# Performance work log

Hardware: AMD Instinct MI355X
Metric: run time of the kernel (lower is better)

The kernel has to match this reference:

```python
import jax, jax.numpy as jnp
import numpy as np

B, T, D, H = 4, 2048, 1024, 16
HS = D // H
EPS = 1e-5

def layer_norm(x, g, b):
    mu = jnp.mean(x, axis=-1, keepdims=True)
    var = jnp.var(x, axis=-1, keepdims=True)
    return (x - mu) * jax.lax.rsqrt(var + EPS) * g + b

def setup_inputs() -> dict:
    key = jax.random.key(0)
    ks = jax.random.split(key, 12)
    s_in = 1.0 / np.sqrt(D)
    s_ff = 1.0 / np.sqrt(4 * D)
    return {
        "x": jax.random.normal(ks[0], (B, T, D), jnp.float32),
        "Wq": jax.random.uniform(ks[1], (H, D, HS), jnp.float32, -s_in, s_in),
        "Wk": jax.random.uniform(ks[2], (H, D, HS), jnp.float32, -s_in, s_in),
        "Wv": jax.random.uniform(ks[3], (H, D, HS), jnp.float32, -s_in, s_in),
        "Wp": jax.random.uniform(ks[4], (D, D), jnp.float32, -s_in, s_in),
        "bp": jax.random.uniform(ks[5], (D,), jnp.float32, -s_in, s_in),
        "W1": jax.random.uniform(ks[6], (D, 4 * D), jnp.float32, -s_in, s_in),
        "b1": jax.random.uniform(ks[7], (4 * D,), jnp.float32, -s_in, s_in),
        "W2": jax.random.uniform(ks[8], (4 * D, D), jnp.float32, -s_ff, s_ff),
        "b2": jax.random.uniform(ks[9], (D,), jnp.float32, -s_ff, s_ff),
        "g1": jnp.ones((D,), jnp.float32),
        "be1": jnp.zeros((D,), jnp.float32),
        "g2": jnp.ones((D,), jnp.float32),
        "be2": jnp.zeros((D,), jnp.float32),
    }

def reference(x, Wq, Wk, Wv, Wp, bp, W1, b1, W2, b2, g1, be1, g2, be2):
    # pre-LN (note: residual uses the NORMALIZED tensor, matching original code)
    h = layer_norm(x, g1, be1)                          # [B,T,D]
    q = jnp.einsum('btd,hdk->bhtk', h, Wq)              # [B,H,T,hs]
    k = jnp.einsum('btd,hdk->bhtk', h, Wk)
    v = jnp.einsum('btd,hdk->bhtk', h, Wv)
    # NOTE: original scales by embedding_size**-0.5, not head_size
    scores = jnp.einsum('bhtk,bhsk->bhts', q, k) * (D ** -0.5)
    causal = jnp.tril(jnp.ones((T, T), bool))
    scores = jnp.where(causal, scores, -jnp.inf)
    att = jax.nn.softmax(scores, axis=-1)               # [B,H,T,T]
    o = jnp.einsum('bhts,bhsk->bhtk', att, v)
    o = o.transpose(0, 2, 1, 3).reshape(B, T, D)        # concat heads
    o = o @ Wp + bp
    x2 = h + o
    h2 = layer_norm(x2, g2, be2)
    ff = jax.nn.relu(h2 @ W1 + b1) @ W2 + b2
    return h2 + ff
```

## Files before the change

kernel.cpp:

```cpp
#include <hip/hip_runtime.h>
#include <hip/hip_bf16.h>

#define Bq 4
#define Tq 2048
#define Dq 1024
#define Hq 16
#define HSq 64
#define EPSq 1e-5f

typedef __attribute__((ext_vector_type(8))) short s16x8;
typedef __attribute__((ext_vector_type(4))) float f32x4;

#define GLL16(g, l)                                                        \
    __builtin_amdgcn_global_load_lds(                                      \
        (const __attribute__((address_space(1))) void*)(g),                \
        (__attribute__((address_space(3))) void*)(l), 16, 0, 0)

__device__ __forceinline__ ushort f2bf(float f) {
    union { float f; unsigned u; } x; x.f = f;
    unsigned r = x.u + 0x7fffu + ((x.u >> 16) & 1u);
    return (ushort)(r >> 16);
}

__global__ __launch_bounds__(256) void ln_bf16(const float* __restrict__ x,
                                               const float* __restrict__ g,
                                               const float* __restrict__ bb,
                                               float* __restrict__ y,
                                               ushort* __restrict__ y16) {
    __shared__ float sdata[8];
    int row = blockIdx.x;
    const float4* xr = (const float4*)(x + (size_t)row * Dq);
    float4 v = xr[threadIdx.x];
    float s  = v.x + v.y + v.z + v.w;
    float ss = v.x*v.x + v.y*v.y + v.z*v.z + v.w*v.w;
    for (int off = 32; off; off >>= 1) {
        s  += __shfl_down(s,  off);
        ss += __shfl_down(ss, off);
    }
    int lane = threadIdx.x & 63, wid = threadIdx.x >> 6;
    if (lane == 0) { sdata[wid] = s; sdata[4 + wid] = ss; }
    __syncthreads();
    if (threadIdx.x == 0) {
        sdata[0] = sdata[0] + sdata[1] + sdata[2] + sdata[3];
        sdata[4] = sdata[4] + sdata[5] + sdata[6] + sdata[7];
    }
    __syncthreads();
    float mu  = sdata[0] * (1.f / Dq);
    float var = sdata[4] * (1.f / Dq) - mu * mu;
    float inv = rsqrtf(var + EPSq);
    float4 gv = ((const float4*)g)[threadIdx.x];
    float4 bv = ((const float4*)bb)[threadIdx.x];
    float4 o;
    o.x = (v.x - mu) * inv * gv.x + bv.x;
    o.y = (v.y - mu) * inv * gv.y + bv.y;
    o.z = (v.z - mu) * inv * gv.z + bv.z;
    o.w = (v.w - mu) * inv * gv.w + bv.w;
    ((float4*)(y + (size_t)row * Dq))[threadIdx.x] = o;
    ushort4 u4;
    u4.x = f2bf(o.x); u4.y = f2bf(o.y); u4.z = f2bf(o.z); u4.w = f2bf(o.w);
    *(ushort4*)(y16 + (size_t)row * Dq + threadIdx.x * 4) = u4;
}

__global__ __launch_bounds__(256) void repack_qkvT(const float* __restrict__ Wqm,
                                                   const float* __restrict__ Wkm,
                                                   const float* __restrict__ Wvm,
                                                   ushort* __restrict__ out) {
    __shared__ float tile[64][65];
    int bid = blockIdx.x;
    int p  = bid >> 8;
    int hh = (bid >> 4) & 15;
    int kt = bid & 15;
    int k0 = kt * 64;
    const float* W = (p == 0) ? Wqm : ((p == 1) ? Wkm : Wvm);
    float scale = (p == 0) ? 0.03125f : 1.0f;
    int j  = threadIdx.x & 63;
    int i0 = threadIdx.x >> 6;
#pragma unroll
    for (int r = 0; r < 16; r++) {
        int i = r * 4 + i0;
        tile[i][j] = W[(size_t)hh * (Dq * HSq) + (size_t)(k0 + i) * HSq + j];
    }
    __syncthreads();
#pragma unroll
    for (int r = 0; r < 16; r++) {
        int i = r * 4 + i0;
        out[(size_t)(p * Dq + hh * HSq + i) * Dq + k0 + j] = f2bf(tile[j][i] * scale);
    }
}

__global__ __launch_bounds__(256) void transpose_cvt(const float* __restrict__ in,
                                                     ushort* __restrict__ out,
                                                     int K, int N) {
    __shared__ float tile[64][65];
    int k0 = blockIdx.y * 64, n0 = blockIdx.x * 64;
    int j  = threadIdx.x & 63;
    int i0 = threadIdx.x >> 6;
#pragma unroll
    for (int r = 0; r < 16; r++) {
        int i = r * 4 + i0;
        tile[i][j] = in[(size_t)(k0 + i) * N + n0 + j];
    }
    __syncthreads();
#pragma unroll
    for (int r = 0; r < 16; r++) {
        int i = r * 4 + i0;
        out[(size_t)(n0 + i) * K + k0 + j] = f2bf(tile[j][i]);
    }
}

template<int BNF>
__global__ __launch_bounds__(256, (BNF == 8) ? 2 : 4)
void gemm_bf16(const ushort* __restrict__ A,
               const ushort* __restrict__ BT,
               const float* __restrict__ bias,
               const float* __restrict__ resid,
               void* __restrict__ Cp,
               ushort* __restrict__ vtg,
               int M, int N, int K,
               int lda, int ldc,
               int relu, int out_bf16,
               int sr) {
    constexpr int BN = BNF * 32;
    constexpr int BSLOT = BN * 32;
    __shared__ ushort lds[2 * 4096 + 3 * BSLOT];
    ushort* Alds = lds;
    ushort* Blds = lds + 2 * 4096;

    int tid = threadIdx.x;
    int w = tid >> 6, lane = tid & 63;
    int lm = lane & 15, quad = lane >> 4;
    int wm = w >> 1, wn = w & 1;

    int bid = blockIdx.x;
    int mtiles = M >> 7, ntiles = N / BN;
    int rt, ct;
    if (mtiles == 64 && (gridDim.x & 7) == 0) {
        int xcd = bid & 7, l = bid >> 3;
        int band = l / (sr * ntiles);
        int rem  = l - band * sr * ntiles;
        ct = rem / sr;
        int srt = rem - ct * sr;
        rt = xcd * 8 + band * sr + srt;
    } else {
        rt = bid % mtiles; ct = bid / mtiles;
    }
    int row0 = rt << 7, col0 = ct * BN;

    int srow = w * 16 + (lane >> 2);
    int schk = (lane & 3) ^ ((lane >> 3) & 3);
    const ushort* pA = A  + (size_t)(row0 + srow) * lda + schk * 8;
    const ushort* pB = BT + (size_t)(col0 + srow) * K  + schk * 8;

    auto stageA = [&](int slot, int t) {
        GLL16(pA + (size_t)t * 32, Alds + slot * 4096 + w * 512);
        GLL16(pA + (size_t)t * 32 + (size_t)64 * lda, Alds + slot * 4096 + 2048 + w * 512);
    };
    auto stageBh = [&](int slot, int t, int h) {
        const ushort* g = pB + (size_t)t * 32 + (size_t)(h * 128) * K;
        ushort* l = Blds + slot * BSLOT + h * 4096 + w * 512;
        GLL16(g, l);
        GLL16(g + (size_t)64 * K, l + 2048);
    };

    int qsw = (quad ^ ((lm >> 1) & 3)) * 8;

    f32x4 zero = {0.f, 0.f, 0.f, 0.f};
    f32x4 acc[4][BNF];
#pragma unroll
    for (int i = 0; i < 4; i++)
#pragma unroll
        for (int jj = 0; jj < BNF; jj++) acc[i][jj] = zero;

    int nkt = K >> 5;

    stageA(0, 0);
    stageBh(0, 0, 0);
    if constexpr (BNF == 8) stageBh(0, 0, 1);
    stageBh(1, 1, 0);
    if constexpr (BNF == 8) stageBh(1, 1, 1);
    __builtin_amdgcn_sched_barrier(0);
    if constexpr (BNF == 8) { asm volatile("s_waitcnt vmcnt(4)" ::: "memory"); }
    else                    { asm volatile("s_waitcnt vmcnt(2)" ::: "memory"); }
    __builtin_amdgcn_s_barrier();
    __builtin_amdgcn_sched_barrier(0);

    int sA = 0, sB = 0;
    for (int t = 0; t < nkt; ++t) {
        const bool stA = (t + 1 < nkt);
        const bool stB = (t + 2 < nkt);
        int sB2 = sB + 2; if (sB2 >= 3) sB2 -= 3;
        const ushort* Ab = Alds + sA * 4096  + (wm * 64 + lm) * 32;
        const ushort* Bb = Blds + sB * BSLOT + (wn * (BNF * 16) + lm) * 32;
        s16x8 a[4], b0[BNF / 2], b1[BNF / 2];

        if (stA) stageA(sA ^ 1, t + 1);
        if (stB) {
            stageBh(sB2, t + 2, 0);
            if constexpr (BNF == 8) stageBh(sB2, t + 2, 1);
        }
        __builtin_amdgcn_sched_barrier(0);

#pragma unroll
        for (int m = 0; m < 4; m++)
            a[m] = *(const s16x8*)(Ab + m * 512 + qsw);
#pragma unroll
        for (int nf = 0; nf < BNF / 2; nf++)
            b0[nf] = *(const s16x8*)(Bb + nf * 512 + qsw);
        __builtin_amdgcn_s_setprio(1);
#pragma unroll
        for (int m = 0; m < 4; m++)
#pragma unroll
            for (int nf = 0; nf < BNF / 2; nf++)
                acc[m][nf] = __builtin_amdgcn_mfma_f32_16x16x32_bf16(a[m], b0[nf], acc[m][nf], 0, 0, 0);
#pragma unroll
        for (int nf = 0; nf < BNF / 2; nf++)
            b1[nf] = *(const s16x8*)(Bb + (nf + BNF / 2) * 512 + qsw);
#pragma unroll
        for (int m = 0; m < 4; m++)
#pragma unroll
            for (int nf = 0; nf < BNF / 2; nf++)
                acc[m][nf + BNF / 2] = __builtin_amdgcn_mfma_f32_16x16x32_bf16(a[m], b1[nf], acc[m][nf + BNF / 2], 0, 0, 0);
        __builtin_amdgcn_s_setprio(0);

        __builtin_amdgcn_sched_barrier(0);
        if (stB) {
            if constexpr (BNF == 8) { asm volatile("s_waitcnt vmcnt(4)" ::: "memory"); }
            else                    { asm volatile("s_waitcnt vmcnt(2)" ::: "memory"); }
        } else if (stA) {
            asm volatile("s_waitcnt vmcnt(0)" ::: "memory");
        }
        if (stA) {
            __builtin_amdgcn_s_barrier();
            __builtin_amdgcn_sched_barrier(0);
        }

        sA ^= 1;
        sB += 1; if (sB >= 3) sB -= 3;
    }

    if (vtg && col0 >= 2048) {
#pragma unroll
        for (int m = 0; m < 4; m++) {
            int r0 = row0 + wm * 64 + m * 16 + quad * 4;
            int bb = r0 >> 11;
            int t  = r0 & (Tq - 1);
#pragma unroll
            for (int nf = 0; nf < BNF; nf++) {
                int hsg = col0 - 2048 + wn * (BNF * 16) + nf * 16 + lm;
                ushort4 u;
                u.x = f2bf(acc[m][nf][0]);
                u.y = f2bf(acc[m][nf][1]);
                u.z = f2bf(acc[m][nf][2]);
                u.w = f2bf(acc[m][nf][3]);
                *(ushort4*)(vtg + ((size_t)(bb * Hq + (hsg >> 6)) * HSq + (hsg & 63)) * Tq + t) = u;
            }
        }
        return;
    }

    float bcol[BNF];
#pragma unroll
    for (int nf = 0; nf < BNF; nf++)
        bcol[nf] = bias ? bias[col0 + wn * (BNF * 16) + nf * 16 + lm] : 0.f;

#pragma unroll
    for (int m = 0; m < 4; m++) {
#pragma unroll
        for (int p = 0; p < 4; p++) {
            int r = row0 + wm * 64 + m * 16 + quad * 4 + p;
#pragma unroll
            for (int nf = 0; nf < BNF; nf++) {
                int cc = col0 + wn * (BNF * 16) + nf * 16 + lm;
                float v = acc[m][nf][p] + bcol[nf];
                if (relu) v = fmaxf(v, 0.f);
                if (resid) v += resid[(size_t)r * ldc + cc];
                if (out_bf16) ((ushort*)Cp)[(size_t)r * ldc + cc] = f2bf(v);
                else          ((float*)Cp)[(size_t)r * ldc + cc] = v;
            }
        }
    }
}

__global__ __launch_bounds__(256) void attn_mfma(const ushort* __restrict__ qkv,
                                                 const ushort* __restrict__ VtG,
                                                 ushort* __restrict__ o16) {
    __shared__ ushort Ks[64 * 72];
    __shared__ ushort Vt[64 * 64];
    __shared__ ushort Ps[4 * 16 * 72];

    int gid = blockIdx.x;
    int b  = gid >> 8;
    int hh = (gid >> 4) & 15;
    int pr = (gid + 7 * b) & 15;
    int qa = pr;
    int qb = 31 - pr;

    int tid = threadIdx.x;
    int w = tid >> 6, lane = tid & 63;
    int lm = lane & 15, quad = lane >> 4;

    const int rs3 = 3 * Dq;
    const ushort* qbase = qkv + (size_t)(b * Tq) * rs3 + hh * HSq;
    int qra = qa * 64 + w * 16 + lm;
    int qrb = qb * 64 + w * 16 + lm;
    s16x8 aqa0 = *(const s16x8*)(qbase + (size_t)qra * rs3 + quad * 8);
    s16x8 aqa1 = *(const s16x8*)(qbase + (size_t)qra * rs3 + 32 + quad * 8);
    s16x8 aqb0 = *(const s16x8*)(qbase + (size_t)qrb * rs3 + quad * 8);
    s16x8 aqb1 = *(const s16x8*)(qbase + (size_t)qrb * rs3 + 32 + quad * 8);

    s16x8 ones;
#pragma unroll
    for (int j = 0; j < 8; j++) ones[j] = (short)0x3F80;

    f32x4 zero = {0.f, 0.f, 0.f, 0.f};
    f32x4 oa[4], ob[4];
#pragma unroll
    for (int nt = 0; nt < 4; nt++) { oa[nt] = zero; ob[nt] = zero; }
    f32x4 la = zero, lb = zero;

    const ushort* kbase = qkv + (size_t)(b * Tq) * rs3 + Dq + hh * HSq;
    const ushort* vtb = VtG + (size_t)((b * Hq + hh) * HSq) * Tq;

    int kr = tid >> 3, kc = (tid & 7) * 8;
    int vh = tid >> 2, vc0 = (tid & 3) * 8;
    int vswz = (((vh >> 3) ^ vh) & 7) << 3;

    s16x8 kp0 = *(const s16x8*)(kbase + (size_t)kr * rs3 + kc);
    s16x8 kp1 = *(const s16x8*)(kbase + (size_t)(kr + 32) * rs3 + kc);
    s16x8 vp0 = *(const s16x8*)(vtb + (size_t)vh * Tq + vc0);
    s16x8 vp1 = *(const s16x8*)(vtb + (size_t)vh * Tq + vc0 + 32);

    auto do_tile = [&](const s16x8& aq0, const s16x8& aq1,
                       f32x4 (&o_acc)[4], f32x4& l_acc, int diag) {
        f32x4 sacc[4];
#pragma unroll
        for (int kt2 = 0; kt2 < 4; kt2++) {
            const ushort* krp = &Ks[(kt2 * 16 + lm) * 72 + quad * 8];
            s16x8 bk0 = *(const s16x8*)krp;
            s16x8 bk1 = *(const s16x8*)(krp + 32);
            f32x4 t = __builtin_amdgcn_mfma_f32_16x16x32_bf16(aq0, bk0, zero, 0, 0, 0);
            sacc[kt2] = __builtin_amdgcn_mfma_f32_16x16x32_bf16(aq1, bk1, t, 0, 0, 0);
        }
        if (diag) {
#pragma unroll
            for (int kt2 = 0; kt2 < 4; kt2++)
#pragma unroll
                for (int r = 0; r < 4; r++)
                    if (kt2 * 16 + lm > w * 16 + quad * 4 + r) sacc[kt2][r] = -1e30f;
        }
#pragma unroll
        for (int kt2 = 0; kt2 < 4; kt2++)
#pragma unroll
            for (int r = 0; r < 4; r++)
                Ps[(w * 16 + quad * 4 + r) * 72 + kt2 * 16 + lm] = f2bf(__expf(sacc[kt2][r]));

        s16x8 ap0 = *(const s16x8*)&Ps[(w * 16 + lm) * 72 + quad * 8];
        s16x8 ap1 = *(const s16x8*)&Ps[(w * 16 + lm) * 72 + 32 + quad * 8];

#pragma unroll
        for (int nt = 0; nt < 4; nt++) {
            int n = nt * 16 + lm;
            int swz = (((n >> 3) ^ n) & 7) << 3;
            s16x8 bv0 = *(const s16x8*)&Vt[n * 64 + ((quad * 8) ^ swz)];
            s16x8 bv1 = *(const s16x8*)&Vt[n * 64 + ((32 + quad * 8) ^ swz)];
            f32x4 t = __builtin_amdgcn_mfma_f32_16x16x32_bf16(ap0, bv0, o_acc[nt], 0, 0, 0);
            o_acc[nt] = __builtin_amdgcn_mfma_f32_16x16x32_bf16(ap1, bv1, t, 0, 0, 0);
        }
        f32x4 t2 = __builtin_amdgcn_mfma_f32_16x16x32_bf16(ap0, ones, l_acc, 0, 0, 0);
        l_acc = __builtin_amdgcn_mfma_f32_16x16x32_bf16(ap1, ones, t2, 0, 0, 0);
    };

    for (int kt = 0; kt <= qb; kt++) {
        __syncthreads();
        *(s16x8*)&Ks[kr * 72 + kc] = kp0;
        *(s16x8*)&Ks[(kr + 32) * 72 + kc] = kp1;
        *(s16x8*)&Vt[vh * 64 + (vc0 ^ vswz)] = vp0;
        *(s16x8*)&Vt[vh * 64 + ((vc0 + 32) ^ vswz)] = vp1;
        __syncthreads();

        if (kt < qb) {
            const ushort* kb = kbase + (size_t)((kt + 1) * 64) * rs3;
            kp0 = *(const s16x8*)(kb + (size_t)kr * rs3 + kc);
            kp1 = *(const s16x8*)(kb + (size_t)(kr + 32) * rs3 + kc);
            const ushort* vb = vtb + (size_t)vh * Tq + (kt + 1) * 64;
            vp0 = *(const s16x8*)(vb + vc0);
            vp1 = *(const s16x8*)(vb + vc0 + 32);
        }

        do_tile(aqb0, aqb1, ob, lb, kt == qb);
        if (kt <= qa)
            do_tile(aqa0, aqa1, oa, la, kt == qa);
    }

#pragma unroll
    for (int r = 0; r < 4; r++) {
        float inva = 1.f / la[r];
        float invb = 1.f / lb[r];
        size_t rowa = (size_t)(b * Tq + qa * 64 + w * 16 + quad * 4 + r);
        size_t rowb = (size_t)(b * Tq + qb * 64 + w * 16 + quad * 4 + r);
#pragma unroll
        for (int nt = 0; nt < 4; nt++) {
            o16[rowa * Dq + hh * HSq + nt * 16 + lm] = f2bf(oa[nt][r] * inva);
            o16[rowb * Dq + hh * HSq + nt * 16 + lm] = f2bf(ob[nt][r] * invb);
        }
    }
}

extern "C" void kernel_launch(void* const* d_in, const int* in_sizes, int n_in,
                              void* d_out, int out_size, void* d_ws, size_t ws_size,
                              hipStream_t stream) {
    const float* x   = (const float*)d_in[0];
    const float* Wq  = (const float*)d_in[1];
    const float* Wk  = (const float*)d_in[2];
    const float* Wv  = (const float*)d_in[3];
    const float* Wp  = (const float*)d_in[4];
    const float* bp  = (const float*)d_in[5];
    const float* W1  = (const float*)d_in[6];
    const float* b1  = (const float*)d_in[7];
    const float* W2  = (const float*)d_in[8];
    const float* b2  = (const float*)d_in[9];
    const float* g1  = (const float*)d_in[10];
    const float* be1 = (const float*)d_in[11];
    const float* g2  = (const float*)d_in[12];
    const float* be2 = (const float*)d_in[13];
    float* out = (float*)d_out;

    const size_t MB = 1u << 20;
    char* ws = (char*)d_ws;
    float*  slotA = (float*)(ws);
    ushort* qkv   = (ushort*)(ws + 32 * MB);
    float*  pbuf  = (float*)(ws + 32 * MB);
    ushort* u16   = (ushort*)(ws + 32 * MB);
    ushort* slotC = (ushort*)(ws + 96 * MB);
    ushort* WqkvT = (ushort*)(ws + 112 * MB);
    ushort* WpT   = (ushort*)(ws + 118 * MB);
    ushort* W1T   = (ushort*)(ws + 120 * MB);
    ushort* W2T   = (ushort*)(ws + 128 * MB);
    ushort* VtG   = (ushort*)(ws + 136 * MB);

    const int rows = Bq * Tq;

    hipLaunchKernelGGL(repack_qkvT, dim3(3 * 16 * 16), dim3(256), 0, stream, Wq, Wk, Wv, WqkvT);
    hipLaunchKernelGGL(transpose_cvt, dim3(Dq / 64, Dq / 64), dim3(256), 0, stream, Wp, WpT, Dq, Dq);
    hipLaunchKernelGGL(transpose_cvt, dim3(4 * Dq / 64, Dq / 64), dim3(256), 0, stream, W1, W1T, Dq, 4 * Dq);
    hipLaunchKernelGGL(transpose_cvt, dim3(Dq / 64, 4 * Dq / 64), dim3(256), 0, stream, W2, W2T, 4 * Dq, Dq);

    hipLaunchKernelGGL(ln_bf16, dim3(rows), dim3(256), 0, stream, x, g1, be1, slotA, slotC);
    hipLaunchKernelGGL(gemm_bf16<8>, dim3((rows / 128) * (3 * Dq / 256)), dim3(256), 0, stream,
                       slotC, WqkvT, (const float*)nullptr, (const float*)nullptr, (void*)qkv, VtG,
                       rows, 3 * Dq, Dq, Dq, 3 * Dq, 0, 1, 8);
    hipLaunchKernelGGL(attn_mfma, dim3(Bq * Hq * 16), dim3(256), 0, stream, qkv, VtG, slotC);
    hipLaunchKernelGGL(gemm_bf16<4>, dim3((rows / 128) * (Dq / 128)), dim3(256), 0, stream,
                       slotC, WpT, bp, slotA, (void*)pbuf, (ushort*)nullptr,
                       rows, Dq, Dq, Dq, Dq, 0, 0, 8);
    hipLaunchKernelGGL(ln_bf16, dim3(rows), dim3(256), 0, stream, pbuf, g2, be2, slotA, slotC);
    hipLaunchKernelGGL(gemm_bf16<8>, dim3((rows / 128) * (4 * Dq / 256)), dim3(256), 0, stream,
                       slotC, W1T, b1, (const float*)nullptr, (void*)u16, (ushort*)nullptr,
                       rows, 4 * Dq, Dq, Dq, 4 * Dq, 1, 1, 8);
    hipLaunchKernelGGL(gemm_bf16<4>, dim3((rows / 128) * (Dq / 128)), dim3(256), 0, stream,
                       u16, W2T, b2, slotA, (void*)out, (ushort*)nullptr,
                       rows, Dq, 4 * Dq, 4 * Dq, Dq, 0, 0, 4);
}
```

Baseline: 503.7 us.

## Process two query-tile pairs per 512-thread attention block sharing K/V tiles

Each attention workgroup now has 8 waves split into two groups. Each group handles its own pair of query tiles (pr/31-pr and 15-pr/16+pr), and both groups share every K/V tile staged in LDS. This halves the grid and the global K/V loads per query, and each thread loads one vector of K and one of V per step instead of two. The cost is imbalance: the group with the shorter pair sits idle at the block barriers while the other finishes, and the larger block may reduce occupancy.

```diff
diff --git a/kernel.cpp b/kernel.cpp
--- a/kernel.cpp
+++ b/kernel.cpp
@@ -281,28 +281,31 @@
     }
 }
 
-__global__ __launch_bounds__(256) void attn_mfma(const ushort* __restrict__ qkv,
+__global__ __launch_bounds__(512) void attn_mfma(const ushort* __restrict__ qkv,
                                                  const ushort* __restrict__ VtG,
                                                  ushort* __restrict__ o16) {
     __shared__ ushort Ks[64 * 72];
     __shared__ ushort Vt[64 * 64];
-    __shared__ ushort Ps[4 * 16 * 72];
+    __shared__ ushort Ps[8 * 16 * 72];
 
     int gid = blockIdx.x;
-    int b  = gid >> 8;
-    int hh = (gid >> 4) & 15;
-    int pr = (gid + 7 * b) & 15;
-    int qa = pr;
-    int qb = 31 - pr;
+    int b  = gid >> 7;
+    int hh = (gid >> 3) & 15;
+    int pr = (gid + 3 * b) & 7;
 
     int tid = threadIdx.x;
     int w = tid >> 6, lane = tid & 63;
+    int g = w >> 2, wl = w & 3;
     int lm = lane & 15, quad = lane >> 4;
+
+    int qa = g ? (15 - pr) : pr;
+    int qb = g ? (16 + pr) : (31 - pr);
+    int qbmax = 31 - pr;
 
     const int rs3 = 3 * Dq;
     const ushort* qbase = qkv + (size_t)(b * Tq) * rs3 + hh * HSq;
-    int qra = qa * 64 + w * 16 + lm;
-    int qrb = qb * 64 + w * 16 + lm;
+    int qra = qa * 64 + wl * 16 + lm;
+    int qrb = qb * 64 + wl * 16 + lm;
     s16x8 aqa0 = *(const s16x8*)(qbase + (size_t)qra * rs3 + quad * 8);
     s16x8 aqa1 = *(const s16x8*)(qbase + (size_t)qra * rs3 + 32 + quad * 8);
     s16x8 aqb0 = *(const s16x8*)(qbase + (size_t)qrb * rs3 + quad * 8);
@@ -322,13 +325,11 @@
     const ushort* vtb = VtG + (size_t)((b * Hq + hh) * HSq) * Tq;
 
     int kr = tid >> 3, kc = (tid & 7) * 8;
-    int vh = tid >> 2, vc0 = (tid & 3) * 8;
+    int vh = tid >> 3, vc0 = (tid & 7) * 8;
     int vswz = (((vh >> 3) ^ vh) & 7) << 3;
 
-    s16x8 kp0 = *(const s16x8*)(kbase + (size_t)kr * rs3 + kc);
-    s16x8 kp1 = *(const s16x8*)(kbase + (size_t)(kr + 32) * rs3 + kc);
-    s16x8 vp0 = *(const s16x8*)(vtb + (size_t)vh * Tq + vc0);
-    s16x8 vp1 = *(const s16x8*)(vtb + (size_t)vh * Tq + vc0 + 32);
+    s16x8 kp = *(const s16x8*)(kbase + (size_t)kr * rs3 + kc);
+    s16x8 vp = *(const s16x8*)(vtb + (size_t)vh * Tq + vc0);
 
     auto do_tile = [&](const s16x8& aq0, const s16x8& aq1,
                        f32x4 (&o_acc)[4], f32x4& l_acc, int diag) {
@@ -346,7 +347,7 @@
             for (int kt2 = 0; kt2 < 4; kt2++)
 #pragma unroll
                 for (int r = 0; r < 4; r++)
-                    if (kt2 * 16 + lm > w * 16 + quad * 4 + r) sacc[kt2][r] = -1e30f;
+                    if (kt2 * 16 + lm > wl * 16 + quad * 4 + r) sacc[kt2][r] = -1e30f;
         }
 #pragma unroll
         for (int kt2 = 0; kt2 < 4; kt2++)
@@ -370,34 +371,27 @@
         l_acc = __builtin_amdgcn_mfma_f32_16x16x32_bf16(ap1, ones, t2, 0, 0, 0);
     };
 
-    for (int kt = 0; kt <= qb; kt++) {
+    for (int kt = 0; kt <= qbmax; kt++) {
         __syncthreads();
-        *(s16x8*)&Ks[kr * 72 + kc] = kp0;
-        *(s16x8*)&Ks[(kr + 32) * 72 + kc] = kp1;
-        *(s16x8*)&Vt[vh * 64 + (vc0 ^ vswz)] = vp0;
-        *(s16x8*)&Vt[vh * 64 + ((vc0 + 32) ^ vswz)] = vp1;
+        *(s16x8*)&Ks[kr * 72 + kc] = kp;
+        *(s16x8*)&Vt[vh * 64 + (vc0 ^ vswz)] = vp;
         __syncthreads();
 
-        if (kt < qb) {
-            const ushort* kb = kbase + (size_t)((kt + 1) * 64) * rs3;
-            kp0 = *(const s16x8*)(kb + (size_t)kr * rs3 + kc);
-            kp1 = *(const s16x8*)(kb + (size_t)(kr + 32) * rs3 + kc);
-            const ushort* vb = vtb + (size_t)vh * Tq + (kt + 1) * 64;
-            vp0 = *(const s16x8*)(vb + vc0);
-            vp1 = *(const s16x8*)(vb + vc0 + 32);
-        }
-
-        do_tile(aqb0, aqb1, ob, lb, kt == qb);
-        if (kt <= qa)
-            do_tile(aqa0, aqa1, oa, la, kt == qa);
+        if (kt < qbmax) {
+            kp = *(const s16x8*)(kbase + (size_t)((kt + 1) * 64 + kr) * rs3 + kc);
+            vp = *(const s16x8*)(vtb + (size_t)vh * Tq + (kt + 1) * 64 + vc0);
+        }
+
+        if (kt <= qb) do_tile(aqb0, aqb1, ob, lb, kt == qb);
+        if (kt <= qa) do_tile(aqa0, aqa1, oa, la, kt == qa);
     }
 
 #pragma unroll
     for (int r = 0; r < 4; r++) {
         float inva = 1.f / la[r];
         float invb = 1.f / lb[r];
-        size_t rowa = (size_t)(b * Tq + qa * 64 + w * 16 + quad * 4 + r);
-        size_t rowb = (size_t)(b * Tq + qb * 64 + w * 16 + quad * 4 + r);
+        size_t rowa = (size_t)(b * Tq + qa * 64 + wl * 16 + quad * 4 + r);
+        size_t rowb = (size_t)(b * Tq + qb * 64 + wl * 16 + quad * 4 + r);
 #pragma unroll
         for (int nt = 0; nt < 4; nt++) {
             o16[rowa * Dq + hh * HSq + nt * 16 + lm] = f2bf(oa[nt][r] * inva);
@@ -449,7 +443,7 @@
     hipLaunchKernelGGL(gemm_bf16<8>, dim3((rows / 128) * (3 * Dq / 256)), dim3(256), 0, stream,
                        slotC, WqkvT, (const float*)nullptr, (const float*)nullptr, (void*)qkv, VtG,
                        rows, 3 * Dq, Dq, Dq, 3 * Dq, 0, 1, 8);
-    hipLaunchKernelGGL(attn_mfma, dim3(Bq * Hq * 16), dim3(256), 0, stream, qkv, VtG, slotC);
+    hipLaunchKernelGGL(attn_mfma, dim3(Bq * Hq * 8), dim3(512), 0, stream, qkv, VtG, slotC);
     hipLaunchKernelGGL(gemm_bf16<4>, dim3((rows / 128) * (Dq / 128)), dim3(256), 0, stream,
                        slotC, WpT, bp, slotA, (void*)pbuf, (ushort*)nullptr,
                        rows, Dq, Dq, Dq, Dq, 0, 0, 8);
```

Measured after the change: 508.0 us. No clear change (+0.9%).

## Add 64-row GEMM kernel with triple-buffered B for N=1024 projections

Applied to the files above, without the earlier changes.

Adds a new 128-thread GEMM kernel with 64x128 output tiles, double-buffered A and triple-buffered B in LDS, XCD-aware tile mapping and swizzled LDS reads. It is used for the attention output projection and the FFN down projection, whose N=1024 outputs gave few 128x128 tiles. Halving the tile height doubles the block count to fill more CUs and adds deeper prefetch. The cost is less operand reuse per tile and more total global traffic for the weight operand.

```diff
diff --git a/kernel.cpp b/kernel.cpp
--- a/kernel.cpp
+++ b/kernel.cpp
@@ -271,6 +271,146 @@
 #pragma unroll
             for (int nf = 0; nf < BNF; nf++) {
                 int cc = col0 + wn * (BNF * 16) + nf * 16 + lm;
+                float v = acc[m][nf][p] + bcol[nf];
+                if (relu) v = fmaxf(v, 0.f);
+                if (resid) v += resid[(size_t)r * ldc + cc];
+                if (out_bf16) ((ushort*)Cp)[(size_t)r * ldc + cc] = f2bf(v);
+                else          ((float*)Cp)[(size_t)r * ldc + cc] = v;
+            }
+        }
+    }
+}
+
+__global__ __launch_bounds__(128, 2)
+void gemm_bm64(const ushort* __restrict__ A,
+               const ushort* __restrict__ BT,
+               const float* __restrict__ bias,
+               const float* __restrict__ resid,
+               void* __restrict__ Cp,
+               int M, int N, int K,
+               int lda, int ldc,
+               int relu, int out_bf16,
+               int sr) {
+    __shared__ ushort lds[2 * 2048 + 3 * 4096];
+    ushort* Alds = lds;
+    ushort* Blds = lds + 2 * 2048;
+
+    int tid = threadIdx.x;
+    int w = tid >> 6, lane = tid & 63;
+    int lm = lane & 15, quad = lane >> 4;
+    int wn = w;
+
+    int bid = blockIdx.x;
+    int mtiles = M >> 6, ntiles = N >> 7;
+    int rt, ct;
+    if ((mtiles & 7) == 0 && (gridDim.x & 7) == 0) {
+        int rpx = mtiles >> 3;
+        int xcd = bid & 7, l = bid >> 3;
+        int band = l / (sr * ntiles);
+        int rem  = l - band * sr * ntiles;
+        ct = rem / sr;
+        int srt = rem - ct * sr;
+        rt = xcd * rpx + band * sr + srt;
+    } else {
+        rt = bid % mtiles; ct = bid / mtiles;
+    }
+    int row0 = rt << 6, col0 = ct << 7;
+
+    int srow = w * 16 + (lane >> 2);
+    int schk = (lane & 3) ^ ((lane >> 3) & 3);
+    const ushort* pA = A  + (size_t)(row0 + srow) * lda + schk * 8;
+    const ushort* pB = BT + (size_t)(col0 + srow) * K  + schk * 8;
+
+    auto stageA = [&](int slot, int t) {
+        GLL16(pA + (size_t)t * 32, Alds + slot * 2048 + w * 512);
+        GLL16(pA + (size_t)t * 32 + (size_t)32 * lda, Alds + slot * 2048 + 1024 + w * 512);
+    };
+    auto stageB = [&](int slot, int t) {
+#pragma unroll
+        for (int s = 0; s < 4; s++)
+            GLL16(pB + (size_t)t * 32 + (size_t)(s * 32) * K,
+                  Blds + slot * 4096 + s * 1024 + w * 512);
+    };
+
+    int qsw = (quad ^ ((lm >> 1) & 3)) * 8;
+
+    f32x4 zero = {0.f, 0.f, 0.f, 0.f};
+    f32x4 acc[4][4];
+#pragma unroll
+    for (int i = 0; i < 4; i++)
+#pragma unroll
+        for (int jj = 0; jj < 4; jj++) acc[i][jj] = zero;
+
+    int nkt = K >> 5;
+
+    stageA(0, 0);
+    stageB(0, 0);
+    stageB(1, 1);
+    __builtin_amdgcn_sched_barrier(0);
+    asm volatile("s_waitcnt vmcnt(4)" ::: "memory");
+    __builtin_amdgcn_s_barrier();
+    __builtin_amdgcn_sched_barrier(0);
+
+    int sA = 0, sB = 0;
+    for (int t = 0; t < nkt; ++t) {
+        const bool stA = (t + 1 < nkt);
+        const bool stB = (t + 2 < nkt);
+        int sB2 = sB + 2; if (sB2 >= 3) sB2 -= 3;
+        const ushort* Ab = Alds + sA * 2048 + lm * 32;
+        const ushort* Bb = Blds + sB * 4096 + (wn * 64 + lm) * 32;
+        s16x8 a[4], b0[2], b1[2];
+
+        if (stA) stageA(sA ^ 1, t + 1);
+        if (stB) stageB(sB2, t + 2);
+        __builtin_amdgcn_sched_barrier(0);
+
+#pragma unroll
+        for (int m = 0; m < 4; m++)
+            a[m] = *(const s16x8*)(Ab + m * 512 + qsw);
+#pragma unroll
+        for (int nf = 0; nf < 2; nf++)
+            b0[nf] = *(const s16x8*)(Bb + nf * 512 + qsw);
+        __builtin_amdgcn_s_setprio(1);
+#pragma unroll
+        for (int m = 0; m < 4; m++)
+#pragma unroll
+            for (int nf = 0; nf < 2; nf++)
+                acc[m][nf] = __builtin_amdgcn_mfma_f32_16x16x32_bf16(a[m], b0[nf], acc[m][nf], 0, 0, 0);
+#pragma unroll
+        for (int nf = 0; nf < 2; nf++)
+            b1[nf] = *(const s16x8*)(Bb + (nf + 2) * 512 + qsw);
+#pragma unroll
+        for (int m = 0; m < 4; m++)
+#pragma unroll
+            for (int nf = 0; nf < 2; nf++)
+                acc[m][nf + 2] = __builtin_amdgcn_mfma_f32_16x16x32_bf16(a[m], b1[nf], acc[m][nf + 2], 0, 0, 0);
+        __builtin_amdgcn_s_setprio(0);
+
+        __builtin_amdgcn_sched_barrier(0);
+        if (stB)      { asm volatile("s_waitcnt vmcnt(4)" ::: "memory"); }
+        else if (stA) { asm volatile("s_waitcnt vmcnt(0)" ::: "memory"); }
+        if (stA) {
+            __builtin_amdgcn_s_barrier();
+            __builtin_amdgcn_sched_barrier(0);
+        }
+
+        sA ^= 1;
+        sB += 1; if (sB >= 3) sB -= 3;
+    }
+
+    float bcol[4];
+#pragma unroll
+    for (int nf = 0; nf < 4; nf++)
+        bcol[nf] = bias ? bias[col0 + wn * 64 + nf * 16 + lm] : 0.f;
+
+#pragma unroll
+    for (int m = 0; m < 4; m++) {
+#pragma unroll
+        for (int p = 0; p < 4; p++) {
+            int r = row0 + m * 16 + quad * 4 + p;
+#pragma unroll
+            for (int nf = 0; nf < 4; nf++) {
+                int cc = col0 + wn * 64 + nf * 16 + lm;
                 float v = acc[m][nf][p] + bcol[nf];
                 if (relu) v = fmaxf(v, 0.f);
                 if (resid) v += resid[(size_t)r * ldc + cc];
@@ -450,14 +590,14 @@
                        slotC, WqkvT, (const float*)nullptr, (const float*)nullptr, (void*)qkv, VtG,
                        rows, 3 * Dq, Dq, Dq, 3 * Dq, 0, 1, 8);
     hipLaunchKernelGGL(attn_mfma, dim3(Bq * Hq * 16), dim3(256), 0, stream, qkv, VtG, slotC);
-    hipLaunchKernelGGL(gemm_bf16<4>, dim3((rows / 128) * (Dq / 128)), dim3(256), 0, stream,
-                       slotC, WpT, bp, slotA, (void*)pbuf, (ushort*)nullptr,
+    hipLaunchKernelGGL(gemm_bm64, dim3((rows / 64) * (Dq / 128)), dim3(128), 0, stream,
+                       slotC, WpT, bp, slotA, (void*)pbuf,
                        rows, Dq, Dq, Dq, Dq, 0, 0, 8);
     hipLaunchKernelGGL(ln_bf16, dim3(rows), dim3(256), 0, stream, pbuf, g2, be2, slotA, slotC);
     hipLaunchKernelGGL(gemm_bf16<8>, dim3((rows / 128) * (4 * Dq / 256)), dim3(256), 0, stream,
                        slotC, W1T, b1, (const float*)nullptr, (void*)u16, (ushort*)nullptr,
                        rows, 4 * Dq, Dq, Dq, 4 * Dq, 1, 1, 8);
-    hipLaunchKernelGGL(gemm_bf16<4>, dim3((rows / 128) * (Dq / 128)), dim3(256), 0, stream,
-                       u16, W2T, b2, slotA, (void*)out, (ushort*)nullptr,
+    hipLaunchKernelGGL(gemm_bm64, dim3((rows / 64) * (Dq / 128)), dim3(128), 0, stream,
+                       u16, W2T, b2, slotA, (void*)out,
                        rows, Dq, 4 * Dq, 4 * Dq, Dq, 0, 0, 4);
 }
```

Measured after the change: 558.7 us. 1.11x slower.
